# Performance work log

Hardware: AMD Instinct MI355X
Metric: run time of the kernel (lower is better)

The kernel has to match this reference:

```python
import jax, jax.numpy as jnp
import numpy as np
from jax import lax

# Module hyperparameters (init_kwargs)
FH, FW = 5, 5          # kernel_size
DIL_Y, DIL_X = 2, 2    # kernel_dilation
G = 2                  # num_deform_groups
F = 64                 # filters
K = FH * FW            # kernel taps


def setup_inputs() -> dict:
    key = jax.random.key(0)
    ks = jax.random.split(key, 4)
    B, H, W, C = 4, 128, 128, 32
    volume = jax.random.normal(ks[0], (B, H, W, C), jnp.float32)
    # offset-predicting conv params: offset_num = FH*FW*G*2 = 100 channels
    w_off = jax.random.normal(ks[1], (FH, FW, C, K * 2 * G), jnp.float32) * 0.01
    b_off = jnp.zeros((K * 2 * G,), jnp.float32)
    # deformable conv weights: (taps, in_channels, filters)
    w_dcn = jax.random.normal(ks[2], (K, C, F), jnp.float32) * (1.0 / np.sqrt(K * C))
    b_dcn = jnp.zeros((F,), jnp.float32)
    return {"volume": volume, "w_off": w_off, "b_off": b_off,
            "w_dcn": w_dcn, "b_dcn": b_dcn}


def _deform_conv(volume, w_off, b_off, w_dcn, b_dcn):
    B, H, W, C = volume.shape
    dp_y = DIL_Y * (FH // 2)  # dilated_pad_y
    dp_x = DIL_X * (FW // 2)  # dilated_pad_x

    # 1) dense offset conv (VALID, dilated) -> (B, oh, ow, K*2*G)
    offsets = lax.conv_general_dilated(
        volume, w_off, window_strides=(1, 1), padding='VALID',
        rhs_dilation=(DIL_Y, DIL_X),
        dimension_numbers=('NHWC', 'HWIO', 'NHWC')) + b_off
    oh, ow = offsets.shape[1], offsets.shape[2]
    off = offsets.reshape(B, oh, ow, K, 2, G)  # [..., (dy,dx), group]

    # 2) base sampling grid (stride 1): output pixel centers + dilated taps
    base_y = jnp.arange(dp_y, H - dp_y, dtype=volume.dtype)   # (oh,)
    base_x = jnp.arange(dp_x, W - dp_x, dtype=volume.dtype)   # (ow,)
    kys = jnp.arange(-dp_y, dp_y + 1, DIL_Y, dtype=volume.dtype)
    kxs = jnp.arange(-dp_x, dp_x + 1, DIL_X, dtype=volume.dtype)
    kus, kvs = jnp.meshgrid(kxs, kys)         # (FH, FW) as in source
    kdy = kvs.reshape(-1)                     # (K,)
    kdx = kus.reshape(-1)                     # (K,)

    # sample positions: (B, oh, ow, K, G)
    py = base_y[None, :, None, None, None] + kdy[None, None, None, :, None] + off[..., 0, :]
    px = base_x[None, None, :, None, None] + kdx[None, None, None, :, None] + off[..., 1, :]
    py = jnp.clip(py, 0.0, H - 1.0)
    px = jnp.clip(px, 0.0, W - 1.0)

    # 3) bilinear gather
    y0 = jnp.clip(jnp.floor(py), 0.0, H - 2.0)
    x0 = jnp.clip(jnp.floor(px), 0.0, W - 2.0)
    wy = (py - y0)[..., None]
    wx = (px - x0)[..., None]
    y0i = y0.astype(jnp.int32)
    x0i = x0.astype(jnp.int32)
    bidx = jnp.arange(B)[:, None, None, None, None]

    def gather(yy, xx):
        return volume[bidx, yy, xx]  # (B, oh, ow, K, G, C)

    v00 = gather(y0i, x0i)
    v01 = gather(y0i, x0i + 1)
    v10 = gather(y0i + 1, x0i)
    v11 = gather(y0i + 1, x0i + 1)
    sampled = (v00 * (1 - wy) * (1 - wx) + v01 * (1 - wy) * wx
               + v10 * wy * (1 - wx) + v11 * wy * wx)  # (B, oh, ow, K, G, C)

    # 4) weighted conv; deform groups partition the output filters
    wr = w_dcn.reshape(K, C, G, F // G)
    out = jnp.einsum('bhwkgc,kcgf->bhwgf', sampled, wr).reshape(B, oh, ow, F)
    return out + b_dcn


def reference(volume, w_off, b_off, w_dcn, b_dcn):
    return _deform_conv(volume, w_off, b_off, w_dcn, b_dcn)
```

## Files before the change

### kernel.cpp

```cpp
#include <hip/hip_runtime.h>
#include <hip/hip_bf16.h>
#include <hip/hip_fp16.h>

#define BB 4
#define HH 128
#define WW 128
#define CC 32
#define OH 120
#define OW 120
#define KT 25
#define OFFC 100
#define FF 64
#define NPX 32
#define NTHREADS 512

typedef __attribute__((ext_vector_type(8))) short   s16x8;
typedef __attribute__((ext_vector_type(8))) _Float16 f16x8;
typedef __attribute__((ext_vector_type(2))) _Float16 h2;
typedef __attribute__((ext_vector_type(4))) float   f32x4;

#define WB_ELEMS   (KT * 7 * 64 * 8)
#define WD_ELEMS   (4 * KT * 64 * 8)
#define VOL_UNITS  (BB * HH * WW * CC / 8)
#define VOL_Q      (VOL_UNITS / 4)
#define VOL16_OFF  (WB_ELEMS + WD_ELEMS)

__device__ __forceinline__ short f2h(float x) {
    _Float16 h = (_Float16)x;
    return __builtin_bit_cast(short, h);
}

__global__ __launch_bounds__(256) void repack_kernel(
    const float* __restrict__ volume, const float* __restrict__ w_off,
    const float* __restrict__ w_dcn, short* __restrict__ ws)
{
    int idx = blockIdx.x * 256 + threadIdx.x;
    short* WB  = ws;
    short* WD  = ws + WB_ELEMS;
    short* V16 = ws + VOL16_OFF;
    if (idx < WB_ELEMS) {
        int j = idx & 7, l = (idx >> 3) & 63;
        int tn = idx >> 9;
        int n = tn % 7, t = tn / 7;
        int c = (l >> 4) * 8 + j;
        int oc = n * 16 + (l & 15);
        float v = (oc < OFFC) ? w_off[(t * CC + c) * OFFC + oc] : 0.f;
        WB[idx] = f2h(v);
    } else if (idx < WB_ELEMS + WD_ELEMS) {
        int idx2 = idx - WB_ELEMS;
        int j = idx2 & 7, l = (idx2 >> 3) & 63;
        int nt = idx2 >> 9;
        int t = nt % KT, n = nt / KT;
        int c = (l >> 4) * 8 + j;
        int f = n * 16 + (l & 15);
        WD[idx2] = f2h(w_dcn[(t * CC + c) * FF + f]);
    } else {
        int v0 = idx - (WB_ELEMS + WD_ELEMS);
        if (v0 < VOL_Q) {
            #pragma unroll
            for (int k = 0; k < 4; ++k) {
                size_t v = (size_t)v0 + (size_t)k * VOL_Q;
                const float* src = volume + v * 8;
                float4 q0 = *(const float4*)src;
                float4 q1 = *(const float4*)(src + 4);
                alignas(16) short tmp[8];
                tmp[0] = f2h(q0.x); tmp[1] = f2h(q0.y); tmp[2] = f2h(q0.z); tmp[3] = f2h(q0.w);
                tmp[4] = f2h(q1.x); tmp[5] = f2h(q1.y); tmp[6] = f2h(q1.z); tmp[7] = f2h(q1.w);
                *(s16x8*)&V16[v * 8] = *(const s16x8*)tmp;
            }
        }
    }
}

__global__ __launch_bounds__(512, 4) void dcn_fused(
    const short* __restrict__ ws_ro, const float* __restrict__ b_off,
    const float* __restrict__ b_dcn, float* __restrict__ out)
{
    __shared__ __align__(16) char smem[38528];
    short* patch   = (short*)smem;
    uint4* pos4    = (uint4*)smem;
    float* offtile = (float*)(smem + 25600);
    f32x4* red     = (f32x4*)(smem + 25600);

    const short* WB  = ws_ro;
    const short* WD  = ws_ro + WB_ELEMS;
    const short* V16 = ws_ro + VOL16_OFF;

    const int tid  = threadIdx.x;
    const int lane = tid & 63;
    const int wv   = tid >> 6;
    const int ox0  = blockIdx.x * NPX;
    const int oy   = blockIdx.y;
    const int b    = blockIdx.z;
    const short* Vb = V16 + (size_t)b * (HH * WW * CC);

    for (int i = tid; i < 9 * 40 * 4; i += NTHREADS) {
        int cq = i & 3;
        int xi = (i >> 2) % 40;
        int yi = (i >> 2) / 40;
        int col = ox0 + xi; col = (col < WW) ? col : (WW - 1);
        s16x8 v = *(const s16x8*)&Vb[((size_t)(oy + yi) * WW + col) * CC + cq * 8];
        int u = ((yi * 40 + xi) << 2) + (cq ^ (xi & 3) ^ ((xi >> 2) & 3));
        *(s16x8*)&patch[u * 8] = v;
    }
    __syncthreads();

    if (wv < 7) {
        const int pr = lane & 15, cq = lane >> 4;
        f32x4 a0 = (f32x4){0.f, 0.f, 0.f, 0.f};
        f32x4 a1 = (f32x4){0.f, 0.f, 0.f, 0.f};
        for (int fh = 0; fh < 5; ++fh) {
            #pragma unroll
            for (int fw = 0; fw < 5; ++fw) {
                int t = fh * 5 + fw;
                int x0 = pr + 2 * fw, x1 = x0 + 16;
                f16x8 af0 = *(const f16x8*)&patch[((((2 * fh) * 40 + x0) << 2) + (cq ^ (x0 & 3) ^ ((x0 >> 2) & 3))) * 8];
                f16x8 af1 = *(const f16x8*)&patch[((((2 * fh) * 40 + x1) << 2) + (cq ^ (x1 & 3) ^ ((x1 >> 2) & 3))) * 8];
                f16x8 bf = *(const f16x8*)&WB[(t * 7 + wv) * 512 + lane * 8];
                a0 = __builtin_amdgcn_mfma_f32_16x16x32_f16(af0, bf, a0, 0, 0, 0);
                a1 = __builtin_amdgcn_mfma_f32_16x16x32_f16(af1, bf, a1, 0, 0, 0);
            }
        }
        int col = lane & 15, q = lane >> 4;
        int oc = wv * 16 + col;
        if (oc < OFFC) {
            float bo = b_off[oc];
            #pragma unroll
            for (int r = 0; r < 4; ++r) {
                offtile[(q * 4 + r) * 101 + oc]      = a0[r] + bo;
                offtile[(16 + q * 4 + r) * 101 + oc] = a1[r] + bo;
            }
        }
    }
    __syncthreads();

    for (int item = tid; item < 1600; item += NTHREADS) {
        int p = item & 31, g = (item >> 5) & 1, t = item >> 6;
        int t5 = t / 5, tm5 = t - t5 * 5;
        float dy = offtile[p * 101 + t * 4 + g];
        float dx = offtile[p * 101 + t * 4 + 2 + g];
        float py = (float)(oy + 2 * t5) + dy;
        float px = (float)(ox0 + p + 2 * tm5) + dx;
        py = fminf(fmaxf(py, 0.f), 127.f);
        px = fminf(fmaxf(px, 0.f), 127.f);
        float y0f = fminf(floorf(py), 126.f);
        float x0f = fminf(floorf(px), 126.f);
        float wy = py - y0f, wx = px - x0f;
        int y0 = (int)y0f, x0i = (int)x0f;
        float w00 = (1.f - wy) * (1.f - wx);
        float w01 = (1.f - wy) * wx;
        float w10 = wy * (1.f - wx);
        float w11 = wy * wx;
        unsigned off = (unsigned)((y0 << 12) + (x0i << 5));
        unsigned wlo = ((unsigned)(unsigned short)f2h(w00)) | (((unsigned)(unsigned short)f2h(w01)) << 16);
        unsigned whi = ((unsigned)(unsigned short)f2h(w10)) | (((unsigned)(unsigned short)f2h(w11)) << 16);
        pos4[((t * 2 + g) << 5) + p] = make_uint4(off, wlo, whi, 0u);
    }
    __syncthreads();

    const int mt = wv >> 2, gg = (wv >> 1) & 1, th = wv & 1;
    const int t0 = th ? 13 : 0, t1 = th ? 25 : 13;
    const int p  = mt * 16 + (lane & 15);
    const int cq = lane >> 4;
    const short* vcq = Vb + cq * 8;
    const short* wd0 = WD + ((gg * 2 + 0) * KT) * 512 + lane * 8;
    const short* wd1 = WD + ((gg * 2 + 1) * KT) * 512 + lane * 8;
    f32x4 acc0 = (f32x4){0.f, 0.f, 0.f, 0.f};
    f32x4 acc1 = (f32x4){0.f, 0.f, 0.f, 0.f};

    uint4 pw = pos4[((t0 * 2 + gg) << 5) + p];
    for (int t = t0; t < t1; ++t) {
        int tn = (t + 1 < t1) ? t + 1 : t0;
        uint4 pwN = pos4[((tn * 2 + gg) << 5) + p];

        const short* vb0 = vcq + pw.x;
        uint4 Au = *(const uint4*)(vb0);
        uint4 Bu = *(const uint4*)(vb0 + CC);
        uint4 Cu = *(const uint4*)(vb0 + WW * CC);
        uint4 Du = *(const uint4*)(vb0 + WW * CC + CC);

        unsigned wyv = pw.y, wzv = pw.z;
        unsigned u00 = ((wyv & 0xffffu) << 16) | (wyv & 0xffffu);
        unsigned u01 = (wyv & 0xffff0000u) | (wyv >> 16);
        unsigned u10 = ((wzv & 0xffffu) << 16) | (wzv & 0xffffu);
        unsigned u11 = (wzv & 0xffff0000u) | (wzv >> 16);
        h2 W00 = __builtin_bit_cast(h2, u00);
        h2 W01 = __builtin_bit_cast(h2, u01);
        h2 W10 = __builtin_bit_cast(h2, u10);
        h2 W11 = __builtin_bit_cast(h2, u11);

        alignas(16) unsigned tmpu[4];
        #pragma unroll
        for (int j = 0; j < 4; ++j) {
            h2 a2 = __builtin_bit_cast(h2, ((const unsigned*)&Au)[j]);
            h2 b2 = __builtin_bit_cast(h2, ((const unsigned*)&Bu)[j]);
            h2 c2 = __builtin_bit_cast(h2, ((const unsigned*)&Cu)[j]);
            h2 d2 = __builtin_bit_cast(h2, ((const unsigned*)&Du)[j]);
            h2 r = a2 * W00;
            r = __builtin_elementwise_fma(b2, W01, r);
            r = __builtin_elementwise_fma(c2, W10, r);
            r = __builtin_elementwise_fma(d2, W11, r);
            tmpu[j] = __builtin_bit_cast(unsigned, r);
        }
        f16x8 af = *(const f16x8*)tmpu;
        acc0 = __builtin_amdgcn_mfma_f32_16x16x32_f16(af, *(const f16x8*)&wd0[t * 512], acc0, 0, 0, 0);
        acc1 = __builtin_amdgcn_mfma_f32_16x16x32_f16(af, *(const f16x8*)&wd1[t * 512], acc1, 0, 0, 0);
        pw = pwN;
    }
    __syncthreads();

    if (th) {
        int slot = wv >> 1;
        red[(slot * 2 + 0) * 64 + lane] = acc0;
        red[(slot * 2 + 1) * 64 + lane] = acc1;
    }
    __syncthreads();
    if (!th) {
        int slot = wv >> 1;
        acc0 += red[(slot * 2 + 0) * 64 + lane];
        acc1 += red[(slot * 2 + 1) * 64 + lane];
        int col = lane & 15, q = lane >> 4;
        int f0 = (gg * 2 + 0) * 16 + col;
        int f1 = (gg * 2 + 1) * 16 + col;
        float bd0 = b_dcn[f0], bd1 = b_dcn[f1];
        long pix0 = ((long)b * OH + oy) * OW + ox0;
        #pragma unroll
        for (int r = 0; r < 4; ++r) {
            int pp = mt * 16 + q * 4 + r;
            if (ox0 + pp < OW) {
                out[(pix0 + pp) * FF + f0] = acc0[r] + bd0;
                out[(pix0 + pp) * FF + f1] = acc1[r] + bd1;
            }
        }
    }
}

extern "C" void kernel_launch(void* const* d_in, const int* in_sizes, int n_in,
                              void* d_out, int out_size, void* d_ws, size_t ws_size,
                              hipStream_t stream) {
    const float* volume = (const float*)d_in[0];
    const float* w_off  = (const float*)d_in[1];
    const float* b_off  = (const float*)d_in[2];
    const float* w_dcn  = (const float*)d_in[3];
    const float* b_dcn  = (const float*)d_in[4];
    float* out = (float*)d_out;
    short* ws  = (short*)d_ws;

    int repack_threads = WB_ELEMS + WD_ELEMS + VOL_Q;
    int repack_blocks  = (repack_threads + 255) / 256;
    repack_kernel<<<repack_blocks, 256, 0, stream>>>(volume, w_off, w_dcn, ws);

    dim3 g2((OW + NPX - 1) / NPX, OH, BB);
    dcn_fused<<<g2, NTHREADS, 0, stream>>>(ws, b_off, b_dcn, out);
}
```

Baseline: 153.1 us.

## Stage bilinear samples in shared memory and split MFMA by filter tile

The sampling stage is restructured. All threads now compute bilinear samples cooperatively per tap half and store them in a swizzled shared-memory tile. Each wave then runs MFMA over its own 16-filter tile, so the per-wave duplicate gathers and the cross-wave reduction go away. Offsets are stored as fp16 and the separate position-precompute pass is removed. The volume repack uses one thread per unit instead of four units per thread. Shared memory grows to about 58KB and launch bounds drop to 2 blocks per CU, which lowers occupancy and adds fp16 rounding of offsets.

```diff
diff --git a/kernel.cpp b/kernel.cpp
--- a/kernel.cpp
+++ b/kernel.cpp
@@ -1,5 +1,4 @@
 #include <hip/hip_runtime.h>
-#include <hip/hip_bf16.h>
 #include <hip/hip_fp16.h>
 
 #define BB 4
@@ -14,20 +13,22 @@
 #define NPX 32
 #define NTHREADS 512
 
-typedef __attribute__((ext_vector_type(8))) short   s16x8;
+typedef __attribute__((ext_vector_type(8))) short    s16x8;
 typedef __attribute__((ext_vector_type(8))) _Float16 f16x8;
 typedef __attribute__((ext_vector_type(2))) _Float16 h2;
-typedef __attribute__((ext_vector_type(4))) float   f32x4;
+typedef __attribute__((ext_vector_type(4))) float    f32x4;
 
 #define WB_ELEMS   (KT * 7 * 64 * 8)
 #define WD_ELEMS   (4 * KT * 64 * 8)
 #define VOL_UNITS  (BB * HH * WW * CC / 8)
-#define VOL_Q      (VOL_UNITS / 4)
 #define VOL16_OFF  (WB_ELEMS + WD_ELEMS)
 
 __device__ __forceinline__ short f2h(float x) {
     _Float16 h = (_Float16)x;
     return __builtin_bit_cast(short, h);
+}
+__device__ __forceinline__ float h2f(short x) {
+    return (float)__builtin_bit_cast(_Float16, x);
 }
 
 __global__ __launch_bounds__(256) void repack_kernel(
@@ -55,32 +56,27 @@
         int f = n * 16 + (l & 15);
         WD[idx2] = f2h(w_dcn[(t * CC + c) * FF + f]);
     } else {
-        int v0 = idx - (WB_ELEMS + WD_ELEMS);
-        if (v0 < VOL_Q) {
-            #pragma unroll
-            for (int k = 0; k < 4; ++k) {
-                size_t v = (size_t)v0 + (size_t)k * VOL_Q;
-                const float* src = volume + v * 8;
-                float4 q0 = *(const float4*)src;
-                float4 q1 = *(const float4*)(src + 4);
-                alignas(16) short tmp[8];
-                tmp[0] = f2h(q0.x); tmp[1] = f2h(q0.y); tmp[2] = f2h(q0.z); tmp[3] = f2h(q0.w);
-                tmp[4] = f2h(q1.x); tmp[5] = f2h(q1.y); tmp[6] = f2h(q1.z); tmp[7] = f2h(q1.w);
-                *(s16x8*)&V16[v * 8] = *(const s16x8*)tmp;
-            }
-        }
-    }
-}
-
-__global__ __launch_bounds__(512, 4) void dcn_fused(
+        int v = idx - (WB_ELEMS + WD_ELEMS);
+        if (v < VOL_UNITS) {
+            const float* src = volume + (size_t)v * 8;
+            float4 q0 = *(const float4*)src;
+            float4 q1 = *(const float4*)(src + 4);
+            alignas(16) short tmp[8];
+            tmp[0] = f2h(q0.x); tmp[1] = f2h(q0.y); tmp[2] = f2h(q0.z); tmp[3] = f2h(q0.w);
+            tmp[4] = f2h(q1.x); tmp[5] = f2h(q1.y); tmp[6] = f2h(q1.z); tmp[7] = f2h(q1.w);
+            *(s16x8*)&V16[(size_t)v * 8] = *(const s16x8*)tmp;
+        }
+    }
+}
+
+__global__ __launch_bounds__(512, 2) void dcn_fused(
     const short* __restrict__ ws_ro, const float* __restrict__ b_off,
     const float* __restrict__ b_dcn, float* __restrict__ out)
 {
-    __shared__ __align__(16) char smem[38528];
+    __shared__ __align__(16) char smem[59648];
+    short* samp    = (short*)smem;
     short* patch   = (short*)smem;
-    uint4* pos4    = (uint4*)smem;
-    float* offtile = (float*)(smem + 25600);
-    f32x4* red     = (f32x4*)(smem + 25600);
+    short* offtile = (short*)(smem + 53248);
 
     const short* WB  = ws_ro;
     const short* WD  = ws_ro + WB_ELEMS;
@@ -127,110 +123,107 @@
             float bo = b_off[oc];
             #pragma unroll
             for (int r = 0; r < 4; ++r) {
-                offtile[(q * 4 + r) * 101 + oc]      = a0[r] + bo;
-                offtile[(16 + q * 4 + r) * 101 + oc] = a1[r] + bo;
+                offtile[(q * 4 + r) * 100 + oc]        = f2h(a0[r] + bo);
+                offtile[(16 + q * 4 + r) * 100 + oc]   = f2h(a1[r] + bo);
             }
         }
     }
     __syncthreads();
 
-    for (int item = tid; item < 1600; item += NTHREADS) {
-        int p = item & 31, g = (item >> 5) & 1, t = item >> 6;
-        int t5 = t / 5, tm5 = t - t5 * 5;
-        float dy = offtile[p * 101 + t * 4 + g];
-        float dx = offtile[p * 101 + t * 4 + 2 + g];
-        float py = (float)(oy + 2 * t5) + dy;
-        float px = (float)(ox0 + p + 2 * tm5) + dx;
-        py = fminf(fmaxf(py, 0.f), 127.f);
-        px = fminf(fmaxf(px, 0.f), 127.f);
-        float y0f = fminf(floorf(py), 126.f);
-        float x0f = fminf(floorf(px), 126.f);
-        float wy = py - y0f, wx = px - x0f;
-        int y0 = (int)y0f, x0i = (int)x0f;
-        float w00 = (1.f - wy) * (1.f - wx);
-        float w01 = (1.f - wy) * wx;
-        float w10 = wy * (1.f - wx);
-        float w11 = wy * wx;
-        unsigned off = (unsigned)((y0 << 12) + (x0i << 5));
-        unsigned wlo = ((unsigned)(unsigned short)f2h(w00)) | (((unsigned)(unsigned short)f2h(w01)) << 16);
-        unsigned whi = ((unsigned)(unsigned short)f2h(w10)) | (((unsigned)(unsigned short)f2h(w11)) << 16);
-        pos4[((t * 2 + g) << 5) + p] = make_uint4(off, wlo, whi, 0u);
-    }
-    __syncthreads();
-
-    const int mt = wv >> 2, gg = (wv >> 1) & 1, th = wv & 1;
-    const int t0 = th ? 13 : 0, t1 = th ? 25 : 13;
-    const int p  = mt * 16 + (lane & 15);
-    const int cq = lane >> 4;
-    const short* vcq = Vb + cq * 8;
-    const short* wd0 = WD + ((gg * 2 + 0) * KT) * 512 + lane * 8;
-    const short* wd1 = WD + ((gg * 2 + 1) * KT) * 512 + lane * 8;
-    f32x4 acc0 = (f32x4){0.f, 0.f, 0.f, 0.f};
-    f32x4 acc1 = (f32x4){0.f, 0.f, 0.f, 0.f};
-
-    uint4 pw = pos4[((t0 * 2 + gg) << 5) + p];
-    for (int t = t0; t < t1; ++t) {
-        int tn = (t + 1 < t1) ? t + 1 : t0;
-        uint4 pwN = pos4[((tn * 2 + gg) << 5) + p];
-
-        const short* vb0 = vcq + pw.x;
-        uint4 Au = *(const uint4*)(vb0);
-        uint4 Bu = *(const uint4*)(vb0 + CC);
-        uint4 Cu = *(const uint4*)(vb0 + WW * CC);
-        uint4 Du = *(const uint4*)(vb0 + WW * CC + CC);
-
-        unsigned wyv = pw.y, wzv = pw.z;
-        unsigned u00 = ((wyv & 0xffffu) << 16) | (wyv & 0xffffu);
-        unsigned u01 = (wyv & 0xffff0000u) | (wyv >> 16);
-        unsigned u10 = ((wzv & 0xffffu) << 16) | (wzv & 0xffffu);
-        unsigned u11 = (wzv & 0xffff0000u) | (wzv >> 16);
-        h2 W00 = __builtin_bit_cast(h2, u00);
-        h2 W01 = __builtin_bit_cast(h2, u01);
-        h2 W10 = __builtin_bit_cast(h2, u10);
-        h2 W11 = __builtin_bit_cast(h2, u11);
-
-        alignas(16) unsigned tmpu[4];
-        #pragma unroll
-        for (int j = 0; j < 4; ++j) {
-            h2 a2 = __builtin_bit_cast(h2, ((const unsigned*)&Au)[j]);
-            h2 b2 = __builtin_bit_cast(h2, ((const unsigned*)&Bu)[j]);
-            h2 c2 = __builtin_bit_cast(h2, ((const unsigned*)&Cu)[j]);
-            h2 d2 = __builtin_bit_cast(h2, ((const unsigned*)&Du)[j]);
-            h2 r = a2 * W00;
-            r = __builtin_elementwise_fma(b2, W01, r);
-            r = __builtin_elementwise_fma(c2, W10, r);
-            r = __builtin_elementwise_fma(d2, W11, r);
-            tmpu[j] = __builtin_bit_cast(unsigned, r);
-        }
-        f16x8 af = *(const f16x8*)tmpu;
-        acc0 = __builtin_amdgcn_mfma_f32_16x16x32_f16(af, *(const f16x8*)&wd0[t * 512], acc0, 0, 0, 0);
-        acc1 = __builtin_amdgcn_mfma_f32_16x16x32_f16(af, *(const f16x8*)&wd1[t * 512], acc1, 0, 0, 0);
-        pw = pwN;
-    }
-    __syncthreads();
-
-    if (th) {
-        int slot = wv >> 1;
-        red[(slot * 2 + 0) * 64 + lane] = acc0;
-        red[(slot * 2 + 1) * 64 + lane] = acc1;
-    }
-    __syncthreads();
-    if (!th) {
-        int slot = wv >> 1;
-        acc0 += red[(slot * 2 + 0) * 64 + lane];
-        acc1 += red[(slot * 2 + 1) * 64 + lane];
+    const int mt = wv & 1;
+    const int ft = wv >> 1;
+    const int g_ = ft >> 1;
+    const int p_ = mt * 16 + (lane & 15);
+    const int cq_ = lane >> 4;
+    f32x4 acc = (f32x4){0.f, 0.f, 0.f, 0.f};
+
+    for (int h = 0; h < 2; ++h) {
+        const int tbase = h ? 13 : 0;
+        const int ntap  = h ? 12 : 13;
+
+        for (int u = tid; u < ntap * 256; u += NTHREADS) {
+            int c  = u & 3;
+            int p  = (u >> 2) & 31;
+            int gg = (u >> 7) & 1;
+            int tp = u >> 8;
+            int t  = tbase + tp;
+            int pe = (ox0 + p < OW) ? p : (OW - 1 - ox0);
+            int t5 = t / 5, tm5 = t - t5 * 5;
+            float dy = h2f(offtile[pe * 100 + t * 4 + gg]);
+            float dx = h2f(offtile[pe * 100 + t * 4 + 2 + gg]);
+            float py = (float)(oy + 2 * t5) + dy;
+            float px = (float)(ox0 + pe + 2 * tm5) + dx;
+            py = fminf(fmaxf(py, 0.f), 127.f);
+            px = fminf(fmaxf(px, 0.f), 127.f);
+            float y0f = fminf(floorf(py), 126.f);
+            float x0f = fminf(floorf(px), 126.f);
+            float wy = py - y0f, wx = px - x0f;
+            int y0 = (int)y0f, x0i = (int)x0f;
+            float w00 = (1.f - wy) * (1.f - wx);
+            float w01 = (1.f - wy) * wx;
+            float w10 = wy * (1.f - wx);
+            float w11 = wy * wx;
+            h2 W00 = (h2){(_Float16)w00, (_Float16)w00};
+            h2 W01 = (h2){(_Float16)w01, (_Float16)w01};
+            h2 W10 = (h2){(_Float16)w10, (_Float16)w10};
+            h2 W11 = (h2){(_Float16)w11, (_Float16)w11};
+
+            const short* vb0 = Vb + ((size_t)(y0 * WW + x0i)) * CC + c * 8;
+            uint4 Au = *(const uint4*)(vb0);
+            uint4 Bu = *(const uint4*)(vb0 + CC);
+            uint4 Cu = *(const uint4*)(vb0 + WW * CC);
+            uint4 Du = *(const uint4*)(vb0 + WW * CC + CC);
+
+            uint4 res;
+            {
+                h2 r0 = __builtin_bit_cast(h2, Au.x) * W00;
+                r0 = __builtin_elementwise_fma(__builtin_bit_cast(h2, Bu.x), W01, r0);
+                r0 = __builtin_elementwise_fma(__builtin_bit_cast(h2, Cu.x), W10, r0);
+                r0 = __builtin_elementwise_fma(__builtin_bit_cast(h2, Du.x), W11, r0);
+                res.x = __builtin_bit_cast(unsigned, r0);
+                h2 r1 = __builtin_bit_cast(h2, Au.y) * W00;
+                r1 = __builtin_elementwise_fma(__builtin_bit_cast(h2, Bu.y), W01, r1);
+                r1 = __builtin_elementwise_fma(__builtin_bit_cast(h2, Cu.y), W10, r1);
+                r1 = __builtin_elementwise_fma(__builtin_bit_cast(h2, Du.y), W11, r1);
+                res.y = __builtin_bit_cast(unsigned, r1);
+                h2 r2 = __builtin_bit_cast(h2, Au.z) * W00;
+                r2 = __builtin_elementwise_fma(__builtin_bit_cast(h2, Bu.z), W01, r2);
+                r2 = __builtin_elementwise_fma(__builtin_bit_cast(h2, Cu.z), W10, r2);
+                r2 = __builtin_elementwise_fma(__builtin_bit_cast(h2, Du.z), W11, r2);
+                res.z = __builtin_bit_cast(unsigned, r2);
+                h2 r3 = __builtin_bit_cast(h2, Au.w) * W00;
+                r3 = __builtin_elementwise_fma(__builtin_bit_cast(h2, Bu.w), W01, r3);
+                r3 = __builtin_elementwise_fma(__builtin_bit_cast(h2, Cu.w), W10, r3);
+                r3 = __builtin_elementwise_fma(__builtin_bit_cast(h2, Du.w), W11, r3);
+                res.w = __builtin_bit_cast(unsigned, r3);
+            }
+            int unit = (tp * 32 + p) * 8 + ((gg * 4 + c) ^ (p & 7));
+            *(uint4*)&samp[unit * 8] = res;
+        }
+        __syncthreads();
+
+        {
+            const short* wd = WD + (ft * KT + tbase) * 512 + lane * 8;
+            for (int tp = 0; tp < ntap; ++tp) {
+                int unit = (tp * 32 + p_) * 8 + ((g_ * 4 + cq_) ^ (p_ & 7));
+                f16x8 af = *(const f16x8*)&samp[unit * 8];
+                f16x8 bf = *(const f16x8*)&wd[tp * 512];
+                acc = __builtin_amdgcn_mfma_f32_16x16x32_f16(af, bf, acc, 0, 0, 0);
+            }
+        }
+        __syncthreads();
+    }
+
+    {
         int col = lane & 15, q = lane >> 4;
-        int f0 = (gg * 2 + 0) * 16 + col;
-        int f1 = (gg * 2 + 1) * 16 + col;
-        float bd0 = b_dcn[f0], bd1 = b_dcn[f1];
+        int f = ft * 16 + col;
+        float bd = b_dcn[f];
         long pix0 = ((long)b * OH + oy) * OW + ox0;
         #pragma unroll
         for (int r = 0; r < 4; ++r) {
             int pp = mt * 16 + q * 4 + r;
-            if (ox0 + pp < OW) {
-                out[(pix0 + pp) * FF + f0] = acc0[r] + bd0;
-                out[(pix0 + pp) * FF + f1] = acc1[r] + bd1;
-            }
+            if (ox0 + pp < OW)
+                out[(pix0 + pp) * FF + f] = acc[r] + bd;
         }
     }
 }
@@ -246,7 +239,7 @@
     float* out = (float*)d_out;
     short* ws  = (short*)d_ws;
 
-    int repack_threads = WB_ELEMS + WD_ELEMS + VOL_Q;
+    int repack_threads = WB_ELEMS + WD_ELEMS + VOL_UNITS;
     int repack_blocks  = (repack_threads + 255) / 256;
     repack_kernel<<<repack_blocks, 256, 0, stream>>>(volume, w_off, w_dcn, ws);
 
```

Result: faster. 127.1 us (-17.0%).
